# Kernel optimization log

Hardware: AMD Instinct MI355X
Metric: run time of the kernel (lower is better)

The kernel has to match this reference:

```python
import jax, jax.numpy as jnp
import numpy as np

C = 512
C8 = C // 8  # 64
B, L = 32, 1024


def setup_inputs() -> dict:
    key = jax.random.key(0)
    ks = jax.random.split(key, 8)
    s = 0.05
    return {
        "x": jax.random.normal(ks[0], (B, C, L), dtype=jnp.float32),
        "Wq": jax.random.normal(ks[1], (C8, C), dtype=jnp.float32) * s,
        "bq": jax.random.normal(ks[2], (C8,), dtype=jnp.float32) * s,
        "Wk": jax.random.normal(ks[3], (C8, C), dtype=jnp.float32) * s,
        "bk": jax.random.normal(ks[4], (C8,), dtype=jnp.float32) * s,
        "Wv": jax.random.normal(ks[5], (C, C), dtype=jnp.float32) * s,
        "bv": jax.random.normal(ks[6], (C,), dtype=jnp.float32) * s,
        "gamma": jax.random.normal(ks[7], (1,), dtype=jnp.float32) * s,
    }


def reference(x, Wq, bq, Wk, bk, Wv, bv, gamma):
    # kernel-size-1 Conv1d == per-position matmul over channels
    q = jnp.einsum('dc,bcl->bdl', Wq, x) + bq[None, :, None]  # [B, C8, L]
    k = jnp.einsum('dc,bcl->bdl', Wk, x) + bk[None, :, None]  # [B, C8, L]
    v = jnp.einsum('oc,bcl->bol', Wv, x) + bv[None, :, None]  # [B, C, L]
    # energy[b, l, m] = <q[:, l], k[:, m]>  (no 1/sqrt(d) scaling, as in source)
    energy = jnp.einsum('bdl,bdm->blm', q, k)                 # [B, L, L]
    attention = jax.nn.softmax(energy, axis=-1)               # softmax over m
    # out[b, c, l] = sum_m v[b, c, m] * attention[b, l, m]
    out = jnp.einsum('bcm,blm->bcl', v, attention)            # [B, C, L]
    out = gamma[0] * out + x
    return (out, attention)
```

## Files before the change

### kernel.cpp

```cpp
#include <hip/hip_runtime.h>

typedef __attribute__((ext_vector_type(8))) short short8;
typedef __attribute__((ext_vector_type(4))) float f32x4;

#define B_SZ 32
#define C_IN 512
#define C8V 64
#define LSEQ 1024
#define OUT_ELEMS (B_SZ * C_IN * LSEQ)

__device__ inline unsigned short bf16_rn(float f) {
  unsigned int u = __float_as_uint(f);
  unsigned int r = 0x7FFFu + ((u >> 16) & 1u);
  return (unsigned short)((u + r) >> 16);
}
__device__ inline float bf16_to_f32(unsigned short h) {
  return __uint_as_float(((unsigned int)h) << 16);
}
__device__ inline void split_bf16(float f, unsigned short &hi, unsigned short &lo) {
  hi = bf16_rn(f);
  lo = bf16_rn(f - bf16_to_f32(hi));
}

__global__ __launch_bounds__(256) void split_weights(
    const float* __restrict__ Wq, const float* __restrict__ Wk, const float* __restrict__ Wv,
    unsigned short* __restrict__ Wqh, unsigned short* __restrict__ Wql,
    unsigned short* __restrict__ Wkh, unsigned short* __restrict__ Wkl,
    unsigned short* __restrict__ Wvh)
{
  int i = (blockIdx.x * 256 + threadIdx.x) * 4;
  if (i < 262144) {
    f32x4 f = *(const f32x4*)&Wv[i];
    #pragma unroll
    for (int j = 0; j < 4; ++j) Wvh[i + j] = bf16_rn(f[j]);
  } else if (i < 294912) {
    int k = i - 262144;
    f32x4 f = *(const f32x4*)&Wq[k];
    #pragma unroll
    for (int j = 0; j < 4; ++j) { unsigned short h, l; split_bf16(f[j], h, l); Wqh[k+j] = h; Wql[k+j] = l; }
  } else {
    int k = i - 294912;
    f32x4 f = *(const f32x4*)&Wk[k];
    #pragma unroll
    for (int j = 0; j < 4; ++j) { unsigned short h, l; split_bf16(f[j], h, l); Wkh[k+j] = h; Wkl[k+j] = l; }
  }
}

__global__ __launch_bounds__(256, 2) void qk_proj(
    const float* __restrict__ x,
    const unsigned short* __restrict__ Wqh, const unsigned short* __restrict__ Wql,
    const unsigned short* __restrict__ Wkh, const unsigned short* __restrict__ Wkl,
    const float* __restrict__ bq, const float* __restrict__ bk,
    unsigned short* __restrict__ qh, unsigned short* __restrict__ ql,
    unsigned short* __restrict__ kh, unsigned short* __restrict__ kl)
{
  const int nt = blockIdx.x;
  const int b  = blockIdx.y;
  const int tid = threadIdx.x;
  const int wave = tid >> 6, lane = tid & 63;
  const int wr = wave >> 1, wc = wave & 1;
  const int g = lane >> 4, ln = lane & 15;

  __shared__ char smem[49152];
  unsigned short* Ah = (unsigned short*)smem;
  unsigned short* Al = Ah + 8192;
  unsigned short* Bh = Al + 8192;
  unsigned short* Bl = Bh + 4096;

  const int rb = tid >> 3, jj = tid & 7;
  const int adst0 = rb*64 + ((jj ^ (rb & 7)) << 3);
  const int xl = tid & 63, xkg = (tid >> 6) * 16;
  const int bdst0 = xl*64 + (((xkg >> 3) ^ (xl & 7)) << 3);
  const long xcol = (long)b*C_IN*LSEQ + (long)nt*64 + xl;

  short8 rAh[4], rAl[4];
  float xv[16];
  rAh[0] = *(const short8*)&Wqh[rb*C_IN + jj*8];
  rAh[1] = *(const short8*)&Wqh[(rb+32)*C_IN + jj*8];
  rAh[2] = *(const short8*)&Wkh[rb*C_IN + jj*8];
  rAh[3] = *(const short8*)&Wkh[(rb+32)*C_IN + jj*8];
  rAl[0] = *(const short8*)&Wql[rb*C_IN + jj*8];
  rAl[1] = *(const short8*)&Wql[(rb+32)*C_IN + jj*8];
  rAl[2] = *(const short8*)&Wkl[rb*C_IN + jj*8];
  rAl[3] = *(const short8*)&Wkl[(rb+32)*C_IN + jj*8];
  #pragma unroll
  for (int i = 0; i < 16; ++i) xv[i] = x[xcol + (long)(xkg + i)*LSEQ];

  f32x4 acc[4][2] = {};

  for (int kb = 0; kb < 8; ++kb) {
    __syncthreads();
    #pragma unroll
    for (int j = 0; j < 4; ++j) {
      *(short8*)&Ah[adst0 + j*2048] = rAh[j];
      *(short8*)&Al[adst0 + j*2048] = rAl[j];
    }
    {
      unsigned short hb[16], lb[16];
      #pragma unroll
      for (int i = 0; i < 16; ++i) split_bf16(xv[i], hb[i], lb[i]);
      #pragma unroll
      for (int s2 = 0; s2 < 2; ++s2) {
        int d = xl*64 + ((((xkg >> 3) + s2) ^ (xl & 7)) << 3);
        *(short8*)&Bh[d] = *(const short8*)&hb[s2*8];
        *(short8*)&Bl[d] = *(const short8*)&lb[s2*8];
      }
    }
    __syncthreads();
    if (kb < 7) {
      int ko = (kb+1)*64;
      rAh[0] = *(const short8*)&Wqh[rb*C_IN + ko + jj*8];
      rAh[1] = *(const short8*)&Wqh[(rb+32)*C_IN + ko + jj*8];
      rAh[2] = *(const short8*)&Wkh[rb*C_IN + ko + jj*8];
      rAh[3] = *(const short8*)&Wkh[(rb+32)*C_IN + ko + jj*8];
      rAl[0] = *(const short8*)&Wql[rb*C_IN + ko + jj*8];
      rAl[1] = *(const short8*)&Wql[(rb+32)*C_IN + ko + jj*8];
      rAl[2] = *(const short8*)&Wkl[rb*C_IN + ko + jj*8];
      rAl[3] = *(const short8*)&Wkl[(rb+32)*C_IN + ko + jj*8];
      #pragma unroll
      for (int i = 0; i < 16; ++i) xv[i] = x[xcol + (long)(ko + xkg + i)*LSEQ];
    }
    __builtin_amdgcn_s_setprio(1);
    #pragma unroll
    for (int ks = 0; ks < 2; ++ks) {
      short8 bhf[2], blf[2];
      #pragma unroll
      for (int ni = 0; ni < 2; ++ni) {
        int cr = wc*32 + ni*16 + ln;
        int s = ((ks*4 + g) ^ (cr & 7)) << 3;
        bhf[ni] = *(const short8*)&Bh[cr*64 + s];
        blf[ni] = *(const short8*)&Bl[cr*64 + s];
      }
      #pragma unroll
      for (int mi = 0; mi < 4; ++mi) {
        int ar = wr*64 + mi*16 + ln;
        int s = ((ks*4 + g) ^ (ar & 7)) << 3;
        short8 ahf = *(const short8*)&Ah[ar*64 + s];
        short8 alf = *(const short8*)&Al[ar*64 + s];
        #pragma unroll
        for (int ni = 0; ni < 2; ++ni) {
          acc[mi][ni] = __builtin_amdgcn_mfma_f32_16x16x32_bf16(ahf, bhf[ni], acc[mi][ni], 0,0,0);
          acc[mi][ni] = __builtin_amdgcn_mfma_f32_16x16x32_bf16(ahf, blf[ni], acc[mi][ni], 0,0,0);
          acc[mi][ni] = __builtin_amdgcn_mfma_f32_16x16x32_bf16(alf, bhf[ni], acc[mi][ni], 0,0,0);
        }
      }
    }
    __builtin_amdgcn_s_setprio(0);
  }
  __syncthreads();
  unsigned short* Trh = (unsigned short*)smem;
  unsigned short* Trl = Trh + 64*136;
  #pragma unroll
  for (int mi = 0; mi < 4; ++mi)
    #pragma unroll
    for (int ni = 0; ni < 2; ++ni)
      #pragma unroll
      for (int j = 0; j < 4; ++j) {
        int rloc = wr*64 + mi*16 + g*4 + j;
        int cloc = wc*32 + ni*16 + ln;
        float bias = (rloc < 64) ? bq[rloc] : bk[rloc - 64];
        unsigned short hi, lo; split_bf16(acc[mi][ni][j] + bias, hi, lo);
        Trh[cloc*136 + rloc] = hi;
        Trl[cloc*136 + rloc] = lo;
      }
  __syncthreads();
  #pragma unroll
  for (int i = 0; i < 4; ++i) {
    int idx = tid + i*256;
    int l = idx >> 4, s = idx & 15;
    long row = ((long)b*LSEQ + nt*64 + l) * 64;
    short8 h  = *(const short8*)&Trh[l*136 + s*8];
    short8 lo = *(const short8*)&Trl[l*136 + s*8];
    if (s < 8) { *(short8*)&qh[row + s*8] = h;      *(short8*)&ql[row + s*8] = lo; }
    else       { *(short8*)&kh[row + (s-8)*8] = h;  *(short8*)&kl[row + (s-8)*8] = lo; }
  }
}

__global__ __launch_bounds__(256, 2) void v_proj(
    const float* __restrict__ x,
    const unsigned short* __restrict__ Wvh,
    const float* __restrict__ bv,
    unsigned short* __restrict__ vws)
{
  const int gi = blockIdx.x;
  const int b  = (gi & 7) + 8 * (gi >> 8);
  const int t  = (gi >> 3) & 31;
  const int lt = t & 7, ct = t >> 3;
  const int tid = threadIdx.x;
  const int wave = tid >> 6, lane = tid & 63;
  const int wr = wave >> 1, wc = wave & 1;
  const int g = lane >> 4, ln = lane & 15;

  __shared__ char smem[34816];
  unsigned short* Ahs = (unsigned short*)smem;
  unsigned short* Bhs = Ahs + 8192;

  const int rb = tid >> 3, jj = tid & 7;
  const int adst0 = rb*64 + ((jj ^ (rb & 7)) << 3);
  const long wbase = (long)(ct*128 + rb)*C_IN + jj*8;
  const int xl = tid & 127, xkg = (tid >> 7) * 32;
  const long xcol = (long)b*C_IN*LSEQ + (long)lt*128 + xl;

  short8 rA[4];
  float xv[32];
  #pragma unroll
  for (int j = 0; j < 4; ++j) rA[j] = *(const short8*)&Wvh[wbase + (long)j*32*C_IN];
  #pragma unroll
  for (int i = 0; i < 32; ++i) xv[i] = x[xcol + (long)(xkg + i)*LSEQ];

  f32x4 acc[4][4] = {};

  for (int kb = 0; kb < 8; ++kb) {
    __syncthreads();
    #pragma unroll
    for (int j = 0; j < 4; ++j)
      *(short8*)&Ahs[adst0 + j*2048] = rA[j];
    {
      unsigned short hb[32];
      #pragma unroll
      for (int i = 0; i < 32; ++i) hb[i] = bf16_rn(xv[i]);
      #pragma unroll
      for (int s2 = 0; s2 < 4; ++s2) {
        int d = xl*64 + ((((xkg >> 3) + s2) ^ (xl & 7)) << 3);
        *(short8*)&Bhs[d] = *(const short8*)&hb[s2*8];
      }
    }
    __syncthreads();
    if (kb < 7) {
      int ko = (kb+1)*64;
      #pragma unroll
      for (int j = 0; j < 4; ++j) rA[j] = *(const short8*)&Wvh[wbase + (long)j*32*C_IN + ko];
      #pragma unroll
      for (int i = 0; i < 32; ++i) xv[i] = x[xcol + (long)(ko + xkg + i)*LSEQ];
    }
    __builtin_amdgcn_s_setprio(1);
    #pragma unroll
    for (int ks = 0; ks < 2; ++ks) {
      short8 bf[4];
      #pragma unroll
      for (int ni = 0; ni < 4; ++ni) {
        int cr = wc*64 + ni*16 + ln;
        bf[ni] = *(const short8*)&Bhs[cr*64 + (((ks*4 + g) ^ (cr & 7)) << 3)];
      }
      #pragma unroll
      for (int mi = 0; mi < 4; ++mi) {
        int ar = wr*64 + mi*16 + ln;
        short8 af = *(const short8*)&Ahs[ar*64 + (((ks*4 + g) ^ (ar & 7)) << 3)];
        #pragma unroll
        for (int ni = 0; ni < 4; ++ni)
          acc[mi][ni] = __builtin_amdgcn_mfma_f32_16x16x32_bf16(af, bf[ni], acc[mi][ni], 0,0,0);
      }
    }
    __builtin_amdgcn_s_setprio(0);
  }
  __syncthreads();
  unsigned short* Tr = (unsigned short*)smem;
  #pragma unroll
  for (int mi = 0; mi < 4; ++mi)
    #pragma unroll
    for (int ni = 0; ni < 4; ++ni)
      #pragma unroll
      for (int j = 0; j < 4; ++j) {
        int rloc = wr*64 + mi*16 + g*4 + j;
        int cloc = wc*64 + ni*16 + ln;
        Tr[rloc*136 + cloc] = bf16_rn(acc[mi][ni][j] + bv[ct*128 + rloc]);
      }
  __syncthreads();
  #pragma unroll
  for (int i = 0; i < 8; ++i) {
    int idx = tid + i*256;
    int c = idx >> 4, s = idx & 15;
    *(short8*)&vws[((long)b*C_IN + ct*128 + c)*LSEQ + lt*128 + s*8] =
      *(const short8*)&Tr[c*136 + s*8];
  }
}

__global__ __launch_bounds__(256, 2) void energy_softmax(
    const unsigned short* __restrict__ qh, const unsigned short* __restrict__ ql,
    const unsigned short* __restrict__ kh, const unsigned short* __restrict__ kl,
    float* __restrict__ attn, unsigned short* __restrict__ pbuf)
{
  const int gi = blockIdx.x;
  const int b  = (gi & 7) + 8 * (gi >> 9);
  const int lt = (gi >> 3) & 63;
  const int tid = threadIdx.x;
  const int wave = tid >> 6, lane = tid & 63;
  const int g = lane >> 4, ln = lane & 15;

  __shared__ unsigned short Ksm[16640];
  __shared__ float redM[4][16];
  __shared__ float redS[4][16];
  unsigned short* Kh = Ksm;
  unsigned short* Kl = Ksm + 8192;

  short8 ah[2], al[2];
  {
    long qrow = ((long)b*LSEQ + lt*16 + ln) * 64;
    #pragma unroll
    for (int ks = 0; ks < 2; ++ks) {
      ah[ks] = *(const short8*)&qh[qrow + ks*32 + g*8];
      al[ks] = *(const short8*)&ql[qrow + ks*32 + g*8];
    }
  }

  const int rb = tid >> 3, jj = tid & 7;
  const int dst0 = rb*64 + ((jj ^ (rb & 7)) << 3);
  const long kbase = ((long)b*LSEQ + rb)*64 + jj*8;

  short8 rkh[4], rkl[4];
  #pragma unroll
  for (int j = 0; j < 4; ++j) {
    rkh[j] = *(const short8*)&kh[kbase + j*2048];
    rkl[j] = *(const short8*)&kl[kbase + j*2048];
  }

  f32x4 acc[8][2] = {};
  #pragma unroll
  for (int c = 0; c < 8; ++c) {
    __syncthreads();
    #pragma unroll
    for (int j = 0; j < 4; ++j) {
      *(short8*)&Kh[dst0 + j*2048] = rkh[j];
      *(short8*)&Kl[dst0 + j*2048] = rkl[j];
    }
    __syncthreads();
    if (c < 7) {
      #pragma unroll
      for (int j = 0; j < 4; ++j) {
        rkh[j] = *(const short8*)&kh[kbase + (long)(c+1)*8192 + j*2048];
        rkl[j] = *(const short8*)&kl[kbase + (long)(c+1)*8192 + j*2048];
      }
    }
    __builtin_amdgcn_s_setprio(1);
    #pragma unroll
    for (int fq = 0; fq < 2; ++fq) {
      int mloc = wave*32 + fq*16 + ln;
      #pragma unroll
      for (int ks = 0; ks < 2; ++ks) {
        int s = ((ks*4 + g) ^ (mloc & 7)) << 3;
        short8 bh = *(const short8*)&Kh[mloc*64 + s];
        short8 bl = *(const short8*)&Kl[mloc*64 + s];
        acc[c][fq] = __builtin_amdgcn_mfma_f32_16x16x32_bf16(ah[ks], bh, acc[c][fq], 0,0,0);
        acc[c][fq] = __builtin_amdgcn_mfma_f32_16x16x32_bf16(ah[ks], bl, acc[c][fq], 0,0,0);
        acc[c][fq] = __builtin_amdgcn_mfma_f32_16x16x32_bf16(al[ks], bh, acc[c][fq], 0,0,0);
      }
    }
    __builtin_amdgcn_s_setprio(0);
  }

  float mx[4];
  #pragma unroll
  for (int j = 0; j < 4; ++j) {
    float m = -1e30f;
    #pragma unroll
    for (int c = 0; c < 8; ++c)
      #pragma unroll
      for (int fq = 0; fq < 2; ++fq) m = fmaxf(m, acc[c][fq][j]);
    #pragma unroll
    for (int off = 1; off < 16; off <<= 1) m = fmaxf(m, __shfl_xor(m, off));
    mx[j] = m;
  }
  if (ln == 0) {
    #pragma unroll
    for (int j = 0; j < 4; ++j) redM[wave][g*4+j] = mx[j];
  }
  __syncthreads();
  #pragma unroll
  for (int j = 0; j < 4; ++j) {
    float m = redM[0][g*4+j];
    #pragma unroll
    for (int w = 1; w < 4; ++w) m = fmaxf(m, redM[w][g*4+j]);
    mx[j] = m;
  }
  float sm[4];
  #pragma unroll
  for (int j = 0; j < 4; ++j) {
    float s = 0.f;
    #pragma unroll
    for (int c = 0; c < 8; ++c)
      #pragma unroll
      for (int fq = 0; fq < 2; ++fq) {
        float p = __expf(acc[c][fq][j] - mx[j]);
        acc[c][fq][j] = p;
        s += p;
      }
    #pragma unroll
    for (int off = 1; off < 16; off <<= 1) s += __shfl_xor(s, off);
    sm[j] = s;
  }
  if (ln == 0) {
    #pragma unroll
    for (int j = 0; j < 4; ++j) redS[wave][g*4+j] = sm[j];
  }
  __syncthreads();
  #pragma unroll
  for (int j = 0; j < 4; ++j) {
    float s = redS[0][g*4+j];
    #pragma unroll
    for (int w = 1; w < 4; ++w) s += redS[w][g*4+j];
    sm[j] = 1.0f / s;
  }

  unsigned short* Pb = Ksm;
  __syncthreads();
  #pragma unroll
  for (int c = 0; c < 8; ++c)
    #pragma unroll
    for (int fq = 0; fq < 2; ++fq) {
      int m0 = c*128 + wave*32 + fq*16 + ln;
      #pragma unroll
      for (int j = 0; j < 4; ++j)
        Pb[(g*4+j)*1032 + m0] = bf16_rn(acc[c][fq][j] * sm[j]);
    }
  __syncthreads();
  #pragma unroll
  for (int u = 0; u < 8; ++u) {
    int cid = tid + u*256;
    int row = cid >> 7, col = (cid & 127) * 8;
    short8 v = *(const short8*)&Pb[row*1032 + col];
    long gro = ((long)b*LSEQ + lt*16 + row)*LSEQ + col;
    *(short8*)&pbuf[gro] = v;
    f32x4 f0, f1;
    #pragma unroll
    for (int i = 0; i < 4; ++i) {
      f0[i] = bf16_to_f32((unsigned short)v[i]);
      f1[i] = bf16_to_f32((unsigned short)v[i+4]);
    }
    *(f32x4*)&attn[gro] = f0;
    *(f32x4*)&attn[gro + 4] = f1;
  }
}

__global__ __launch_bounds__(512, 2) void pv_out(
    const unsigned short* __restrict__ vws,
    const unsigned short* __restrict__ pbuf,
    const float* __restrict__ x,
    const float* __restrict__ gamma,
    float* __restrict__ out)
{
  const int gi = blockIdx.x;
  const int b  = (gi & 7) + 8 * (gi >> 7);
  const int t  = (gi >> 3) & 15;
  const int lt = t >> 2, ct = t & 3;
  const int tid = threadIdx.x;
  const int w = tid >> 6, lane = tid & 63;
  const int wcq = w >> 2, wlq = w & 3;
  const int g = lane >> 4, ln = lane & 15;

  __shared__ char smem[49152];
  unsigned short* Vst = (unsigned short*)smem;
  unsigned short* Pst = (unsigned short*)(smem + 16384);

  const int vr = tid >> 2, vs0 = (tid & 3) * 2;
  const long vbase = ((long)b*C_IN + ct*128 + vr)*LSEQ + vs0*8;
  const int pr = tid >> 1, ps0 = (tid & 1) * 4;
  const long pbase = ((long)b*LSEQ + lt*256 + pr)*LSEQ + ps0*8;

  f32x4 acc[4][4] = {};
  short8 rv[2], rp[4];
  #pragma unroll
  for (int j = 0; j < 2; ++j) rv[j] = *(const short8*)&vws[vbase + j*8];
  #pragma unroll
  for (int j = 0; j < 4; ++j) rp[j] = *(const short8*)&pbuf[pbase + j*8];

  for (int mb = 0; mb < 16; ++mb) {
    __syncthreads();
    #pragma unroll
    for (int j = 0; j < 2; ++j)
      *(short8*)&Vst[vr*64 + (((vs0 + j) ^ (vr & 7)) << 3)] = rv[j];
    #pragma unroll
    for (int j = 0; j < 4; ++j)
      *(short8*)&Pst[pr*64 + (((ps0 + j) ^ (pr & 7)) << 3)] = rp[j];
    __syncthreads();
    if (mb < 15) {
      #pragma unroll
      for (int j = 0; j < 2; ++j) rv[j] = *(const short8*)&vws[vbase + (mb+1)*64 + j*8];
      #pragma unroll
      for (int j = 0; j < 4; ++j) rp[j] = *(const short8*)&pbuf[pbase + (mb+1)*64 + j*8];
    }
    __builtin_amdgcn_s_setprio(1);
    #pragma unroll
    for (int ks = 0; ks < 2; ++ks) {
      short8 bf[4];
      #pragma unroll
      for (int lf = 0; lf < 4; ++lf) {
        int prow = wlq*64 + lf*16 + ln;
        bf[lf] = *(const short8*)&Pst[prow*64 + (((ks*4 + g) ^ (prow & 7)) << 3)];
      }
      #pragma unroll
      for (int cf = 0; cf < 4; ++cf) {
        int cr = wcq*64 + cf*16 + ln;
        short8 af = *(const short8*)&Vst[cr*64 + (((ks*4 + g) ^ (cr & 7)) << 3)];
        #pragma unroll
        for (int lf = 0; lf < 4; ++lf)
          acc[cf][lf] = __builtin_amdgcn_mfma_f32_16x16x32_bf16(af, bf[lf], acc[cf][lf], 0,0,0);
      }
    }
    __builtin_amdgcn_s_setprio(0);
  }

  const float gm = gamma[0];
  #pragma unroll
  for (int cf = 0; cf < 4; ++cf)
    #pragma unroll
    for (int lf = 0; lf < 4; ++lf)
      #pragma unroll
      for (int j = 0; j < 4; ++j) {
        int c = ct*128 + wcq*64 + cf*16 + g*4 + j;
        int l = lt*256 + wlq*64 + lf*16 + ln;
        long o = ((long)b*C_IN + c)*LSEQ + l;
        out[o] = gm * acc[cf][lf][j] + x[o];
      }
}

extern "C" void kernel_launch(void* const* d_in, const int* in_sizes, int n_in,
                              void* d_out, int out_size, void* d_ws, size_t ws_size,
                              hipStream_t stream)
{
  const float* x  = (const float*)d_in[0];
  const float* Wq = (const float*)d_in[1];
  const float* bq = (const float*)d_in[2];
  const float* Wk = (const float*)d_in[3];
  const float* bk = (const float*)d_in[4];
  const float* Wv = (const float*)d_in[5];
  const float* bv = (const float*)d_in[6];
  const float* gamma = (const float*)d_in[7];
  float* out  = (float*)d_out;
  float* attn = out + OUT_ELEMS;

  char* ws = (char*)d_ws;
  unsigned short* Wqh = (unsigned short*)(ws + 0);
  unsigned short* Wql = (unsigned short*)(ws + 65536);
  unsigned short* Wkh = (unsigned short*)(ws + 131072);
  unsigned short* Wkl = (unsigned short*)(ws + 196608);
  unsigned short* Wvh = (unsigned short*)(ws + 262144);
  unsigned short* qhp = (unsigned short*)(ws + 786432);
  unsigned short* qlp = (unsigned short*)(ws + 786432 + 1ul*4194304);
  unsigned short* khp = (unsigned short*)(ws + 786432 + 2ul*4194304);
  unsigned short* klp = (unsigned short*)(ws + 786432 + 3ul*4194304);
  unsigned short* vws = (unsigned short*)(ws + 786432 + 4ul*4194304);
  unsigned short* pbuf = (unsigned short*)(ws + 786432 + 4ul*4194304 + 33554432);

  split_weights<<<320, 256, 0, stream>>>(Wq, Wk, Wv, Wqh, Wql, Wkh, Wkl, Wvh);
  qk_proj<<<dim3(16, B_SZ), 256, 0, stream>>>(x, Wqh, Wql, Wkh, Wkl, bq, bk, qhp, qlp, khp, klp);
  v_proj<<<1024, 256, 0, stream>>>(x, Wvh, bv, vws);
  energy_softmax<<<2048, 256, 0, stream>>>(qhp, qlp, khp, klp, attn, pbuf);
  pv_out<<<512, 512, 0, stream>>>(vws, pbuf, x, gamma, out);
}
```

Before: 183.6 us.

## Merge QK and V projections into one launch; double query rows per energy block

The separate qk_proj and v_proj kernels become a single launch in which the first 512 blocks compute Q/K and the remaining 1024 compute V. This removes one launch and lets the two projections overlap on the GPU. The qk branch also remaps its blocks so that neighbouring blocks work on different batches. The energy_softmax kernel now handles 32 query rows per block instead of 16, so each staged K tile is reused twice and the grid is halved. In exchange it needs twice the accumulator registers and about 66 KB of LDS, which may lower occupancy.

```diff
diff --git a/kernel.cpp b/kernel.cpp
--- a/kernel.cpp
+++ b/kernel.cpp
@@ -46,232 +46,226 @@
   }
 }
 
-__global__ __launch_bounds__(256, 2) void qk_proj(
+__global__ __launch_bounds__(256, 2) void proj(
     const float* __restrict__ x,
     const unsigned short* __restrict__ Wqh, const unsigned short* __restrict__ Wql,
     const unsigned short* __restrict__ Wkh, const unsigned short* __restrict__ Wkl,
+    const unsigned short* __restrict__ Wvh,
     const float* __restrict__ bq, const float* __restrict__ bk,
+    const float* __restrict__ bv,
     unsigned short* __restrict__ qh, unsigned short* __restrict__ ql,
-    unsigned short* __restrict__ kh, unsigned short* __restrict__ kl)
+    unsigned short* __restrict__ kh, unsigned short* __restrict__ kl,
+    unsigned short* __restrict__ vws)
 {
-  const int nt = blockIdx.x;
-  const int b  = blockIdx.y;
+  __shared__ char smem[49152];
   const int tid = threadIdx.x;
   const int wave = tid >> 6, lane = tid & 63;
   const int wr = wave >> 1, wc = wave & 1;
   const int g = lane >> 4, ln = lane & 15;
 
-  __shared__ char smem[49152];
-  unsigned short* Ah = (unsigned short*)smem;
-  unsigned short* Al = Ah + 8192;
-  unsigned short* Bh = Al + 8192;
-  unsigned short* Bl = Bh + 4096;
-
-  const int rb = tid >> 3, jj = tid & 7;
-  const int adst0 = rb*64 + ((jj ^ (rb & 7)) << 3);
-  const int xl = tid & 63, xkg = (tid >> 6) * 16;
-  const int bdst0 = xl*64 + (((xkg >> 3) ^ (xl & 7)) << 3);
-  const long xcol = (long)b*C_IN*LSEQ + (long)nt*64 + xl;
-
-  short8 rAh[4], rAl[4];
-  float xv[16];
-  rAh[0] = *(const short8*)&Wqh[rb*C_IN + jj*8];
-  rAh[1] = *(const short8*)&Wqh[(rb+32)*C_IN + jj*8];
-  rAh[2] = *(const short8*)&Wkh[rb*C_IN + jj*8];
-  rAh[3] = *(const short8*)&Wkh[(rb+32)*C_IN + jj*8];
-  rAl[0] = *(const short8*)&Wql[rb*C_IN + jj*8];
-  rAl[1] = *(const short8*)&Wql[(rb+32)*C_IN + jj*8];
-  rAl[2] = *(const short8*)&Wkl[rb*C_IN + jj*8];
-  rAl[3] = *(const short8*)&Wkl[(rb+32)*C_IN + jj*8];
-  #pragma unroll
-  for (int i = 0; i < 16; ++i) xv[i] = x[xcol + (long)(xkg + i)*LSEQ];
-
-  f32x4 acc[4][2] = {};
-
-  for (int kb = 0; kb < 8; ++kb) {
-    __syncthreads();
-    #pragma unroll
-    for (int j = 0; j < 4; ++j) {
-      *(short8*)&Ah[adst0 + j*2048] = rAh[j];
-      *(short8*)&Al[adst0 + j*2048] = rAl[j];
-    }
-    {
-      unsigned short hb[16], lb[16];
-      #pragma unroll
-      for (int i = 0; i < 16; ++i) split_bf16(xv[i], hb[i], lb[i]);
-      #pragma unroll
-      for (int s2 = 0; s2 < 2; ++s2) {
-        int d = xl*64 + ((((xkg >> 3) + s2) ^ (xl & 7)) << 3);
-        *(short8*)&Bh[d] = *(const short8*)&hb[s2*8];
-        *(short8*)&Bl[d] = *(const short8*)&lb[s2*8];
-      }
-    }
-    __syncthreads();
-    if (kb < 7) {
-      int ko = (kb+1)*64;
-      rAh[0] = *(const short8*)&Wqh[rb*C_IN + ko + jj*8];
-      rAh[1] = *(const short8*)&Wqh[(rb+32)*C_IN + ko + jj*8];
-      rAh[2] = *(const short8*)&Wkh[rb*C_IN + ko + jj*8];
-      rAh[3] = *(const short8*)&Wkh[(rb+32)*C_IN + ko + jj*8];
-      rAl[0] = *(const short8*)&Wql[rb*C_IN + ko + jj*8];
-      rAl[1] = *(const short8*)&Wql[(rb+32)*C_IN + ko + jj*8];
-      rAl[2] = *(const short8*)&Wkl[rb*C_IN + ko + jj*8];
-      rAl[3] = *(const short8*)&Wkl[(rb+32)*C_IN + ko + jj*8];
-      #pragma unroll
-      for (int i = 0; i < 16; ++i) xv[i] = x[xcol + (long)(ko + xkg + i)*LSEQ];
-    }
-    __builtin_amdgcn_s_setprio(1);
-    #pragma unroll
-    for (int ks = 0; ks < 2; ++ks) {
-      short8 bhf[2], blf[2];
-      #pragma unroll
-      for (int ni = 0; ni < 2; ++ni) {
-        int cr = wc*32 + ni*16 + ln;
-        int s = ((ks*4 + g) ^ (cr & 7)) << 3;
-        bhf[ni] = *(const short8*)&Bh[cr*64 + s];
-        blf[ni] = *(const short8*)&Bl[cr*64 + s];
-      }
-      #pragma unroll
-      for (int mi = 0; mi < 4; ++mi) {
-        int ar = wr*64 + mi*16 + ln;
-        int s = ((ks*4 + g) ^ (ar & 7)) << 3;
-        short8 ahf = *(const short8*)&Ah[ar*64 + s];
-        short8 alf = *(const short8*)&Al[ar*64 + s];
+  if (blockIdx.x < 512) {
+    const int gi = blockIdx.x;
+    const int b  = (gi & 7) + 8 * (gi >> 7);
+    const int nt = (gi >> 3) & 15;
+
+    unsigned short* Ah = (unsigned short*)smem;
+    unsigned short* Al = Ah + 8192;
+    unsigned short* Bh = Al + 8192;
+    unsigned short* Bl = Bh + 4096;
+
+    const int rb = tid >> 3, jj = tid & 7;
+    const int adst0 = rb*64 + ((jj ^ (rb & 7)) << 3);
+    const int xl = tid & 63, xkg = (tid >> 6) * 16;
+    const long xcol = (long)b*C_IN*LSEQ + (long)nt*64 + xl;
+
+    short8 rAh[4], rAl[4];
+    float xv[16];
+    rAh[0] = *(const short8*)&Wqh[rb*C_IN + jj*8];
+    rAh[1] = *(const short8*)&Wqh[(rb+32)*C_IN + jj*8];
+    rAh[2] = *(const short8*)&Wkh[rb*C_IN + jj*8];
+    rAh[3] = *(const short8*)&Wkh[(rb+32)*C_IN + jj*8];
+    rAl[0] = *(const short8*)&Wql[rb*C_IN + jj*8];
+    rAl[1] = *(const short8*)&Wql[(rb+32)*C_IN + jj*8];
+    rAl[2] = *(const short8*)&Wkl[rb*C_IN + jj*8];
+    rAl[3] = *(const short8*)&Wkl[(rb+32)*C_IN + jj*8];
+    #pragma unroll
+    for (int i = 0; i < 16; ++i) xv[i] = x[xcol + (long)(xkg + i)*LSEQ];
+
+    f32x4 acc[4][2] = {};
+
+    for (int kb = 0; kb < 8; ++kb) {
+      __syncthreads();
+      #pragma unroll
+      for (int j = 0; j < 4; ++j) {
+        *(short8*)&Ah[adst0 + j*2048] = rAh[j];
+        *(short8*)&Al[adst0 + j*2048] = rAl[j];
+      }
+      {
+        unsigned short hb[16], lb[16];
+        #pragma unroll
+        for (int i = 0; i < 16; ++i) split_bf16(xv[i], hb[i], lb[i]);
+        #pragma unroll
+        for (int s2 = 0; s2 < 2; ++s2) {
+          int d = xl*64 + ((((xkg >> 3) + s2) ^ (xl & 7)) << 3);
+          *(short8*)&Bh[d] = *(const short8*)&hb[s2*8];
+          *(short8*)&Bl[d] = *(const short8*)&lb[s2*8];
+        }
+      }
+      __syncthreads();
+      if (kb < 7) {
+        int ko = (kb+1)*64;
+        rAh[0] = *(const short8*)&Wqh[rb*C_IN + ko + jj*8];
+        rAh[1] = *(const short8*)&Wqh[(rb+32)*C_IN + ko + jj*8];
+        rAh[2] = *(const short8*)&Wkh[rb*C_IN + ko + jj*8];
+        rAh[3] = *(const short8*)&Wkh[(rb+32)*C_IN + ko + jj*8];
+        rAl[0] = *(const short8*)&Wql[rb*C_IN + ko + jj*8];
+        rAl[1] = *(const short8*)&Wql[(rb+32)*C_IN + ko + jj*8];
+        rAl[2] = *(const short8*)&Wkl[rb*C_IN + ko + jj*8];
+        rAl[3] = *(const short8*)&Wkl[(rb+32)*C_IN + ko + jj*8];
+        #pragma unroll
+        for (int i = 0; i < 16; ++i) xv[i] = x[xcol + (long)(ko + xkg + i)*LSEQ];
+      }
+      __builtin_amdgcn_s_setprio(1);
+      #pragma unroll
+      for (int ks = 0; ks < 2; ++ks) {
+        short8 bhf[2], blf[2];
         #pragma unroll
         for (int ni = 0; ni < 2; ++ni) {
-          acc[mi][ni] = __builtin_amdgcn_mfma_f32_16x16x32_bf16(ahf, bhf[ni], acc[mi][ni], 0,0,0);
-          acc[mi][ni] = __builtin_amdgcn_mfma_f32_16x16x32_bf16(ahf, blf[ni], acc[mi][ni], 0,0,0);
-          acc[mi][ni] = __builtin_amdgcn_mfma_f32_16x16x32_bf16(alf, bhf[ni], acc[mi][ni], 0,0,0);
-        }
-      }
-    }
-    __builtin_amdgcn_s_setprio(0);
-  }
-  __syncthreads();
-  unsigned short* Trh = (unsigned short*)smem;
-  unsigned short* Trl = Trh + 64*136;
-  #pragma unroll
-  for (int mi = 0; mi < 4; ++mi)
-    #pragma unroll
-    for (int ni = 0; ni < 2; ++ni)
-      #pragma unroll
-      for (int j = 0; j < 4; ++j) {
-        int rloc = wr*64 + mi*16 + g*4 + j;
-        int cloc = wc*32 + ni*16 + ln;
-        float bias = (rloc < 64) ? bq[rloc] : bk[rloc - 64];
-        unsigned short hi, lo; split_bf16(acc[mi][ni][j] + bias, hi, lo);
-        Trh[cloc*136 + rloc] = hi;
-        Trl[cloc*136 + rloc] = lo;
-      }
-  __syncthreads();
-  #pragma unroll
-  for (int i = 0; i < 4; ++i) {
-    int idx = tid + i*256;
-    int l = idx >> 4, s = idx & 15;
-    long row = ((long)b*LSEQ + nt*64 + l) * 64;
-    short8 h  = *(const short8*)&Trh[l*136 + s*8];
-    short8 lo = *(const short8*)&Trl[l*136 + s*8];
-    if (s < 8) { *(short8*)&qh[row + s*8] = h;      *(short8*)&ql[row + s*8] = lo; }
-    else       { *(short8*)&kh[row + (s-8)*8] = h;  *(short8*)&kl[row + (s-8)*8] = lo; }
-  }
-}
-
-__global__ __launch_bounds__(256, 2) void v_proj(
-    const float* __restrict__ x,
-    const unsigned short* __restrict__ Wvh,
-    const float* __restrict__ bv,
-    unsigned short* __restrict__ vws)
-{
-  const int gi = blockIdx.x;
-  const int b  = (gi & 7) + 8 * (gi >> 8);
-  const int t  = (gi >> 3) & 31;
-  const int lt = t & 7, ct = t >> 3;
-  const int tid = threadIdx.x;
-  const int wave = tid >> 6, lane = tid & 63;
-  const int wr = wave >> 1, wc = wave & 1;
-  const int g = lane >> 4, ln = lane & 15;
-
-  __shared__ char smem[34816];
-  unsigned short* Ahs = (unsigned short*)smem;
-  unsigned short* Bhs = Ahs + 8192;
-
-  const int rb = tid >> 3, jj = tid & 7;
-  const int adst0 = rb*64 + ((jj ^ (rb & 7)) << 3);
-  const long wbase = (long)(ct*128 + rb)*C_IN + jj*8;
-  const int xl = tid & 127, xkg = (tid >> 7) * 32;
-  const long xcol = (long)b*C_IN*LSEQ + (long)lt*128 + xl;
-
-  short8 rA[4];
-  float xv[32];
-  #pragma unroll
-  for (int j = 0; j < 4; ++j) rA[j] = *(const short8*)&Wvh[wbase + (long)j*32*C_IN];
-  #pragma unroll
-  for (int i = 0; i < 32; ++i) xv[i] = x[xcol + (long)(xkg + i)*LSEQ];
-
-  f32x4 acc[4][4] = {};
-
-  for (int kb = 0; kb < 8; ++kb) {
-    __syncthreads();
-    #pragma unroll
-    for (int j = 0; j < 4; ++j)
-      *(short8*)&Ahs[adst0 + j*2048] = rA[j];
-    {
-      unsigned short hb[32];
-      #pragma unroll
-      for (int i = 0; i < 32; ++i) hb[i] = bf16_rn(xv[i]);
-      #pragma unroll
-      for (int s2 = 0; s2 < 4; ++s2) {
-        int d = xl*64 + ((((xkg >> 3) + s2) ^ (xl & 7)) << 3);
-        *(short8*)&Bhs[d] = *(const short8*)&hb[s2*8];
-      }
-    }
-    __syncthreads();
-    if (kb < 7) {
-      int ko = (kb+1)*64;
-      #pragma unroll
-      for (int j = 0; j < 4; ++j) rA[j] = *(const short8*)&Wvh[wbase + (long)j*32*C_IN + ko];
-      #pragma unroll
-      for (int i = 0; i < 32; ++i) xv[i] = x[xcol + (long)(ko + xkg + i)*LSEQ];
-    }
-    __builtin_amdgcn_s_setprio(1);
-    #pragma unroll
-    for (int ks = 0; ks < 2; ++ks) {
-      short8 bf[4];
-      #pragma unroll
-      for (int ni = 0; ni < 4; ++ni) {
-        int cr = wc*64 + ni*16 + ln;
-        bf[ni] = *(const short8*)&Bhs[cr*64 + (((ks*4 + g) ^ (cr & 7)) << 3)];
-      }
-      #pragma unroll
-      for (int mi = 0; mi < 4; ++mi) {
-        int ar = wr*64 + mi*16 + ln;
-        short8 af = *(const short8*)&Ahs[ar*64 + (((ks*4 + g) ^ (ar & 7)) << 3)];
-        #pragma unroll
-        for (int ni = 0; ni < 4; ++ni)
-          acc[mi][ni] = __builtin_amdgcn_mfma_f32_16x16x32_bf16(af, bf[ni], acc[mi][ni], 0,0,0);
-      }
-    }
-    __builtin_amdgcn_s_setprio(0);
-  }
-  __syncthreads();
-  unsigned short* Tr = (unsigned short*)smem;
-  #pragma unroll
-  for (int mi = 0; mi < 4; ++mi)
-    #pragma unroll
-    for (int ni = 0; ni < 4; ++ni)
-      #pragma unroll
-      for (int j = 0; j < 4; ++j) {
-        int rloc = wr*64 + mi*16 + g*4 + j;
-        int cloc = wc*64 + ni*16 + ln;
-        Tr[rloc*136 + cloc] = bf16_rn(acc[mi][ni][j] + bv[ct*128 + rloc]);
-      }
-  __syncthreads();
-  #pragma unroll
-  for (int i = 0; i < 8; ++i) {
-    int idx = tid + i*256;
-    int c = idx >> 4, s = idx & 15;
-    *(short8*)&vws[((long)b*C_IN + ct*128 + c)*LSEQ + lt*128 + s*8] =
-      *(const short8*)&Tr[c*136 + s*8];
+          int cr = wc*32 + ni*16 + ln;
+          int s = ((ks*4 + g) ^ (cr & 7)) << 3;
+          bhf[ni] = *(const short8*)&Bh[cr*64 + s];
+          blf[ni] = *(const short8*)&Bl[cr*64 + s];
+        }
+        #pragma unroll
+        for (int mi = 0; mi < 4; ++mi) {
+          int ar = wr*64 + mi*16 + ln;
+          int s = ((ks*4 + g) ^ (ar & 7)) << 3;
+          short8 ahf = *(const short8*)&Ah[ar*64 + s];
+          short8 alf = *(const short8*)&Al[ar*64 + s];
+          #pragma unroll
+          for (int ni = 0; ni < 2; ++ni) {
+            acc[mi][ni] = __builtin_amdgcn_mfma_f32_16x16x32_bf16(ahf, bhf[ni], acc[mi][ni], 0,0,0);
+            acc[mi][ni] = __builtin_amdgcn_mfma_f32_16x16x32_bf16(ahf, blf[ni], acc[mi][ni], 0,0,0);
+            acc[mi][ni] = __builtin_amdgcn_mfma_f32_16x16x32_bf16(alf, bhf[ni], acc[mi][ni], 0,0,0);
+          }
+        }
+      }
+      __builtin_amdgcn_s_setprio(0);
+    }
+    __syncthreads();
+    unsigned short* Trh = (unsigned short*)smem;
+    unsigned short* Trl = Trh + 64*136;
+    #pragma unroll
+    for (int mi = 0; mi < 4; ++mi)
+      #pragma unroll
+      for (int ni = 0; ni < 2; ++ni)
+        #pragma unroll
+        for (int j = 0; j < 4; ++j) {
+          int rloc = wr*64 + mi*16 + g*4 + j;
+          int cloc = wc*32 + ni*16 + ln;
+          float bias = (rloc < 64) ? bq[rloc] : bk[rloc - 64];
+          unsigned short hi, lo; split_bf16(acc[mi][ni][j] + bias, hi, lo);
+          Trh[cloc*136 + rloc] = hi;
+          Trl[cloc*136 + rloc] = lo;
+        }
+    __syncthreads();
+    #pragma unroll
+    for (int i = 0; i < 4; ++i) {
+      int idx = tid + i*256;
+      int l = idx >> 4, s = idx & 15;
+      long row = ((long)b*LSEQ + nt*64 + l) * 64;
+      short8 h  = *(const short8*)&Trh[l*136 + s*8];
+      short8 lo = *(const short8*)&Trl[l*136 + s*8];
+      if (s < 8) { *(short8*)&qh[row + s*8] = h;      *(short8*)&ql[row + s*8] = lo; }
+      else       { *(short8*)&kh[row + (s-8)*8] = h;  *(short8*)&kl[row + (s-8)*8] = lo; }
+    }
+  } else {
+    const int gj = blockIdx.x - 512;
+    const int b  = (gj & 7) + 8 * (gj >> 8);
+    const int t  = (gj >> 3) & 31;
+    const int lt = t & 7, ct = t >> 3;
+
+    unsigned short* Ahs = (unsigned short*)smem;
+    unsigned short* Bhs = Ahs + 8192;
+
+    const int rb = tid >> 3, jj = tid & 7;
+    const int adst0 = rb*64 + ((jj ^ (rb & 7)) << 3);
+    const long wbase = (long)(ct*128 + rb)*C_IN + jj*8;
+    const int xl = tid & 127, xkg = (tid >> 7) * 32;
+    const long xcol = (long)b*C_IN*LSEQ + (long)lt*128 + xl;
+
+    short8 rA[4];
+    float xv[32];
+    #pragma unroll
+    for (int j = 0; j < 4; ++j) rA[j] = *(const short8*)&Wvh[wbase + (long)j*32*C_IN];
+    #pragma unroll
+    for (int i = 0; i < 32; ++i) xv[i] = x[xcol + (long)(xkg + i)*LSEQ];
+
+    f32x4 acc[4][4] = {};
+
+    for (int kb = 0; kb < 8; ++kb) {
+      __syncthreads();
+      #pragma unroll
+      for (int j = 0; j < 4; ++j)
+        *(short8*)&Ahs[adst0 + j*2048] = rA[j];
+      {
+        unsigned short hb[32];
+        #pragma unroll
+        for (int i = 0; i < 32; ++i) hb[i] = bf16_rn(xv[i]);
+        #pragma unroll
+        for (int s2 = 0; s2 < 4; ++s2) {
+          int d = xl*64 + ((((xkg >> 3) + s2) ^ (xl & 7)) << 3);
+          *(short8*)&Bhs[d] = *(const short8*)&hb[s2*8];
+        }
+      }
+      __syncthreads();
+      if (kb < 7) {
+        int ko = (kb+1)*64;
+        #pragma unroll
+        for (int j = 0; j < 4; ++j) rA[j] = *(const short8*)&Wvh[wbase + (long)j*32*C_IN + ko];
+        #pragma unroll
+        for (int i = 0; i < 32; ++i) xv[i] = x[xcol + (long)(ko + xkg + i)*LSEQ];
+      }
+      __builtin_amdgcn_s_setprio(1);
+      #pragma unroll
+      for (int ks = 0; ks < 2; ++ks) {
+        short8 bf[4];
+        #pragma unroll
+        for (int ni = 0; ni < 4; ++ni) {
+          int cr = wc*64 + ni*16 + ln;
+          bf[ni] = *(const short8*)&Bhs[cr*64 + (((ks*4 + g) ^ (cr & 7)) << 3)];
+        }
+        #pragma unroll
+        for (int mi = 0; mi < 4; ++mi) {
+          int ar = wr*64 + mi*16 + ln;
+          short8 af = *(const short8*)&Ahs[ar*64 + (((ks*4 + g) ^ (ar & 7)) << 3)];
+          #pragma unroll
+          for (int ni = 0; ni < 4; ++ni)
+            acc[mi][ni] = __builtin_amdgcn_mfma_f32_16x16x32_bf16(af, bf[ni], acc[mi][ni], 0,0,0);
+        }
+      }
+      __builtin_amdgcn_s_setprio(0);
+    }
+    __syncthreads();
+    unsigned short* Tr = (unsigned short*)smem;
+    #pragma unroll
+    for (int mi = 0; mi < 4; ++mi)
+      #pragma unroll
+      for (int ni = 0; ni < 4; ++ni)
+        #pragma unroll
+        for (int j = 0; j < 4; ++j) {
+          int rloc = wr*64 + mi*16 + g*4 + j;
+          int cloc = wc*64 + ni*16 + ln;
+          Tr[rloc*136 + cloc] = bf16_rn(acc[mi][ni][j] + bv[ct*128 + rloc]);
+        }
+    __syncthreads();
+    #pragma unroll
+    for (int i = 0; i < 8; ++i) {
+      int idx = tid + i*256;
+      int c = idx >> 4, s = idx & 15;
+      *(short8*)&vws[((long)b*C_IN + ct*128 + c)*LSEQ + lt*128 + s*8] =
+        *(const short8*)&Tr[c*136 + s*8];
+    }
   }
 }
 
@@ -281,27 +275,27 @@
     float* __restrict__ attn, unsigned short* __restrict__ pbuf)
 {
   const int gi = blockIdx.x;
-  const int b  = (gi & 7) + 8 * (gi >> 9);
-  const int lt = (gi >> 3) & 63;
+  const int b  = (gi & 7) + 8 * (gi >> 8);
+  const int lt = (gi >> 3) & 31;
   const int tid = threadIdx.x;
   const int wave = tid >> 6, lane = tid & 63;
   const int g = lane >> 4, ln = lane & 15;
 
-  __shared__ unsigned short Ksm[16640];
-  __shared__ float redM[4][16];
-  __shared__ float redS[4][16];
+  __shared__ unsigned short Ksm[33024];
+  __shared__ float redM[4][32];
+  __shared__ float redS[4][32];
   unsigned short* Kh = Ksm;
   unsigned short* Kl = Ksm + 8192;
 
-  short8 ah[2], al[2];
-  {
-    long qrow = ((long)b*LSEQ + lt*16 + ln) * 64;
+  short8 ah[2][2], al[2][2];
+  #pragma unroll
+  for (int li = 0; li < 2; ++li)
     #pragma unroll
     for (int ks = 0; ks < 2; ++ks) {
-      ah[ks] = *(const short8*)&qh[qrow + ks*32 + g*8];
-      al[ks] = *(const short8*)&ql[qrow + ks*32 + g*8];
-    }
-  }
+      long qrow = ((long)b*LSEQ + lt*32 + li*16 + ln) * 64;
+      ah[li][ks] = *(const short8*)&qh[qrow + ks*32 + g*8];
+      al[li][ks] = *(const short8*)&ql[qrow + ks*32 + g*8];
+    }
 
   const int rb = tid >> 3, jj = tid & 7;
   const int dst0 = rb*64 + ((jj ^ (rb & 7)) << 3);
@@ -314,7 +308,7 @@
     rkl[j] = *(const short8*)&kl[kbase + j*2048];
   }
 
-  f32x4 acc[8][2] = {};
+  f32x4 acc[8][2][2] = {};
   #pragma unroll
   for (int c = 0; c < 8; ++c) {
     __syncthreads();
@@ -340,66 +334,81 @@
         int s = ((ks*4 + g) ^ (mloc & 7)) << 3;
         short8 bh = *(const short8*)&Kh[mloc*64 + s];
         short8 bl = *(const short8*)&Kl[mloc*64 + s];
-        acc[c][fq] = __builtin_amdgcn_mfma_f32_16x16x32_bf16(ah[ks], bh, acc[c][fq], 0,0,0);
-        acc[c][fq] = __builtin_amdgcn_mfma_f32_16x16x32_bf16(ah[ks], bl, acc[c][fq], 0,0,0);
-        acc[c][fq] = __builtin_amdgcn_mfma_f32_16x16x32_bf16(al[ks], bh, acc[c][fq], 0,0,0);
+        #pragma unroll
+        for (int li = 0; li < 2; ++li) {
+          acc[c][fq][li] = __builtin_amdgcn_mfma_f32_16x16x32_bf16(ah[li][ks], bh, acc[c][fq][li], 0,0,0);
+          acc[c][fq][li] = __builtin_amdgcn_mfma_f32_16x16x32_bf16(ah[li][ks], bl, acc[c][fq][li], 0,0,0);
+          acc[c][fq][li] = __builtin_amdgcn_mfma_f32_16x16x32_bf16(al[li][ks], bh, acc[c][fq][li], 0,0,0);
+        }
       }
     }
     __builtin_amdgcn_s_setprio(0);
   }
 
-  float mx[4];
-  #pragma unroll
-  for (int j = 0; j < 4; ++j) {
-    float m = -1e30f;
-    #pragma unroll
-    for (int c = 0; c < 8; ++c)
-      #pragma unroll
-      for (int fq = 0; fq < 2; ++fq) m = fmaxf(m, acc[c][fq][j]);
-    #pragma unroll
-    for (int off = 1; off < 16; off <<= 1) m = fmaxf(m, __shfl_xor(m, off));
-    mx[j] = m;
-  }
+  float mx[2][4];
+  #pragma unroll
+  for (int li = 0; li < 2; ++li)
+    #pragma unroll
+    for (int j = 0; j < 4; ++j) {
+      float m = -1e30f;
+      #pragma unroll
+      for (int c = 0; c < 8; ++c)
+        #pragma unroll
+        for (int fq = 0; fq < 2; ++fq) m = fmaxf(m, acc[c][fq][li][j]);
+      #pragma unroll
+      for (int off = 1; off < 16; off <<= 1) m = fmaxf(m, __shfl_xor(m, off));
+      mx[li][j] = m;
+    }
   if (ln == 0) {
     #pragma unroll
-    for (int j = 0; j < 4; ++j) redM[wave][g*4+j] = mx[j];
+    for (int li = 0; li < 2; ++li)
+      #pragma unroll
+      for (int j = 0; j < 4; ++j) redM[wave][li*16 + g*4 + j] = mx[li][j];
   }
   __syncthreads();
   #pragma unroll
-  for (int j = 0; j < 4; ++j) {
-    float m = redM[0][g*4+j];
-    #pragma unroll
-    for (int w = 1; w < 4; ++w) m = fmaxf(m, redM[w][g*4+j]);
-    mx[j] = m;
-  }
-  float sm[4];
-  #pragma unroll
-  for (int j = 0; j < 4; ++j) {
-    float s = 0.f;
-    #pragma unroll
-    for (int c = 0; c < 8; ++c)
-      #pragma unroll
-      for (int fq = 0; fq < 2; ++fq) {
-        float p = __expf(acc[c][fq][j] - mx[j]);
-        acc[c][fq][j] = p;
-        s += p;
-      }
-    #pragma unroll
-    for (int off = 1; off < 16; off <<= 1) s += __shfl_xor(s, off);
-    sm[j] = s;
-  }
+  for (int li = 0; li < 2; ++li)
+    #pragma unroll
+    for (int j = 0; j < 4; ++j) {
+      float m = redM[0][li*16 + g*4 + j];
+      #pragma unroll
+      for (int w = 1; w < 4; ++w) m = fmaxf(m, redM[w][li*16 + g*4 + j]);
+      mx[li][j] = m;
+    }
+  float sm[2][4];
+  #pragma unroll
+  for (int li = 0; li < 2; ++li)
+    #pragma unroll
+    for (int j = 0; j < 4; ++j) {
+      float s = 0.f;
+      #pragma unroll
+      for (int c = 0; c < 8; ++c)
+        #pragma unroll
+        for (int fq = 0; fq < 2; ++fq) {
+          float p = __expf(acc[c][fq][li][j] - mx[li][j]);
+          acc[c][fq][li][j] = p;
+          s += p;
+        }
+      #pragma unroll
+      for (int off = 1; off < 16; off <<= 1) s += __shfl_xor(s, off);
+      sm[li][j] = s;
+    }
   if (ln == 0) {
     #pragma unroll
-    for (int j = 0; j < 4; ++j) redS[wave][g*4+j] = sm[j];
+    for (int li = 0; li < 2; ++li)
+      #pragma unroll
+      for (int j = 0; j < 4; ++j) redS[wave][li*16 + g*4 + j] = sm[li][j];
   }
   __syncthreads();
   #pragma unroll
-  for (int j = 0; j < 4; ++j) {
-    float s = redS[0][g*4+j];
-    #pragma unroll
-    for (int w = 1; w < 4; ++w) s += redS[w][g*4+j];
-    sm[j] = 1.0f / s;
-  }
+  for (int li = 0; li < 2; ++li)
+    #pragma unroll
+    for (int j = 0; j < 4; ++j) {
+      float s = redS[0][li*16 + g*4 + j];
+      #pragma unroll
+      for (int w = 1; w < 4; ++w) s += redS[w][li*16 + g*4 + j];
+      sm[li][j] = 1.0f / s;
+    }
 
   unsigned short* Pb = Ksm;
   __syncthreads();
@@ -409,16 +418,18 @@
     for (int fq = 0; fq < 2; ++fq) {
       int m0 = c*128 + wave*32 + fq*16 + ln;
       #pragma unroll
-      for (int j = 0; j < 4; ++j)
-        Pb[(g*4+j)*1032 + m0] = bf16_rn(acc[c][fq][j] * sm[j]);
+      for (int li = 0; li < 2; ++li)
+        #pragma unroll
+        for (int j = 0; j < 4; ++j)
+          Pb[(li*16 + g*4 + j)*1032 + m0] = bf16_rn(acc[c][fq][li][j] * sm[li][j]);
     }
   __syncthreads();
   #pragma unroll
-  for (int u = 0; u < 8; ++u) {
+  for (int u = 0; u < 16; ++u) {
     int cid = tid + u*256;
     int row = cid >> 7, col = (cid & 127) * 8;
     short8 v = *(const short8*)&Pb[row*1032 + col];
-    long gro = ((long)b*LSEQ + lt*16 + row)*LSEQ + col;
+    long gro = ((long)b*LSEQ + lt*32 + row)*LSEQ + col;
     *(short8*)&pbuf[gro] = v;
     f32x4 f0, f1;
     #pragma unroll
@@ -542,8 +553,7 @@
   unsigned short* pbuf = (unsigned short*)(ws + 786432 + 4ul*4194304 + 33554432);
 
   split_weights<<<320, 256, 0, stream>>>(Wq, Wk, Wv, Wqh, Wql, Wkh, Wkl, Wvh);
-  qk_proj<<<dim3(16, B_SZ), 256, 0, stream>>>(x, Wqh, Wql, Wkh, Wkl, bq, bk, qhp, qlp, khp, klp);
-  v_proj<<<1024, 256, 0, stream>>>(x, Wvh, bv, vws);
-  energy_softmax<<<2048, 256, 0, stream>>>(qhp, qlp, khp, klp, attn, pbuf);
+  proj<<<1536, 256, 0, stream>>>(x, Wqh, Wql, Wkh, Wkl, Wvh, bq, bk, bv, qhp, qlp, khp, klp, vws);
+  energy_softmax<<<1024, 256, 0, stream>>>(qhp, qlp, khp, klp, attn, pbuf);
   pv_out<<<512, 512, 0, stream>>>(vws, pbuf, x, gamma, out);
 }
```

Result: faster. 175.9 us (-4.2%).
